# Kernel optimization log

Hardware: AMD Instinct MI355X
Metric: run time of the kernel (lower is better)

## Reference

```python
import jax, jax.numpy as jnp
import numpy as np

EPS = 1e-5
TEMP = 0.07
LARGE_NEG = -1e9


def mi_net(x, W1, g1, b1, W2, b2, Ws, lng, lnb):
    # x: (B, C, T). 1x1 convs == per-position channel projections.
    y = jnp.einsum('bct,oc->bot', x, W1)                      # conv1 (no bias)
    mu = y.mean(axis=(0, 2), keepdims=True)                   # BatchNorm2d, training-mode batch stats
    var = y.var(axis=(0, 2), keepdims=True)
    y = (y - mu) * jax.lax.rsqrt(var + EPS) * g1[None, :, None] + b1[None, :, None]
    y = jax.nn.relu(y)
    y = jnp.einsum('bot,po->bpt', y, W2) + b2[None, :, None]  # conv2 (bias)
    h = y + jnp.einsum('bct,oc->bot', x, Ws)                  # linear shortcut
    mu2 = h.mean(axis=1, keepdims=True)                       # LayerNorm over channel dim
    v2 = h.var(axis=1, keepdims=True)
    return (h - mu2) * jax.lax.rsqrt(v2 + EPS) * lng[None, :, None] + lnb[None, :, None]


def infonce(L, G):
    # L: (N, D, T) locals, G: (N, D) single global per sample (n_multis = 1)
    N, D, T = L.shape
    l_p = jnp.swapaxes(L, 1, 2)                               # (N, T, D)
    l_p = l_p / jnp.linalg.norm(l_p, axis=2, keepdims=True)
    g = G / jnp.linalg.norm(G, axis=1, keepdims=True)         # (N, D)
    u_p = (jnp.einsum('ntd,nd->nt', l_p, g) / TEMP)[:, :, None]   # (N, T, 1), positives scaled by temp
    # negatives: <global_i, local_{j,t}>; NOT divided by temperature (faithful to torch source)
    u_n = jnp.einsum('nd,mtd->nmt', g, l_p)                   # (N, N, T)
    eye = jnp.eye(N, dtype=bool)[:, :, None]
    u_n = jnp.where(eye, LARGE_NEG, u_n).reshape(N, N * T)    # mask self pairs
    logits = jnp.concatenate(
        [u_p, jnp.broadcast_to(u_n[:, None, :], (N, T, N * T))], axis=2)  # (N, T, 1+N*T)
    logp = jax.nn.log_softmax(logits, axis=2)
    return -logp[:, :, 0].mean()


def setup_inputs() -> dict:
    key = jax.random.key(0)
    ks = jax.random.split(key, 10)
    B, CL, CG, T, MI = 32, 1536, 192, 256, 512
    d = {
        'local_feat': jax.random.normal(ks[0], (B, CL, T), jnp.float32),
        'global_feat': jax.random.normal(ks[1], (B, CG), jnp.float32),
        # local_net params
        'lW1': jax.random.normal(ks[2], (MI, CL), jnp.float32) * 0.02,
        'lg1': jnp.ones((MI,), jnp.float32),
        'lb1': jnp.zeros((MI,), jnp.float32),
        'lW2': jax.random.normal(ks[3], (MI, MI), jnp.float32) * 0.02,
        'lb2': jnp.zeros((MI,), jnp.float32),
        'lWs': jax.random.normal(ks[4], (MI, CL), jnp.float32) * 0.02,
        'llng': jnp.ones((MI,), jnp.float32),
        'llnb': jnp.zeros((MI,), jnp.float32),
        # global_net params (global_channels != mi_units -> net exists)
        'gW1': jax.random.normal(ks[5], (MI, CG), jnp.float32) * 0.02,
        'gg1': jnp.ones((MI,), jnp.float32),
        'gb1': jnp.zeros((MI,), jnp.float32),
        'gW2': jax.random.normal(ks[6], (MI, MI), jnp.float32) * 0.02,
        'gb2': jnp.zeros((MI,), jnp.float32),
    }
    # shortcut with near-identity init (n_units >= n_input for global net)
    gWs = jax.random.uniform(ks[7], (MI, CG), jnp.float32, -0.01, 0.01)
    gWs = gWs.at[jnp.arange(CG), jnp.arange(CG)].set(1.0)
    d['gWs'] = gWs
    d['glng'] = jnp.ones((MI,), jnp.float32)
    d['glnb'] = jnp.zeros((MI,), jnp.float32)
    return d


def reference(local_feat, global_feat,
              lW1, lg1, lb1, lW2, lb2, lWs, llng, llnb,
              gW1, gg1, gb1, gW2, gb2, gWs, glng, glnb):
    L = mi_net(local_feat, lW1, lg1, lb1, lW2, lb2, lWs, llng, llnb)      # (B, MI, T)
    G = mi_net(global_feat[:, :, None], gW1, gg1, gb1, gW2, gb2, gWs, glng, glnb)[:, :, 0]  # (B, MI)
    return infonce(L, G)
```

## Files before the change

### kernel.cpp

```cpp
#include <hip/hip_runtime.h>

#define B 32
#define CL 1536
#define CG 192
#define T 256
#define MI 512
#define NPOS 8192
#define EPS 1e-5f
#define TEMP 0.07f

typedef __attribute__((ext_vector_type(8))) __bf16 bf16x8;
typedef __attribute__((ext_vector_type(4))) float f32x4;

__device__ __forceinline__ unsigned short f2bf(float f) {
  union { float f; unsigned u; } v; v.f = f;
  unsigned r = v.u + 0x7FFFu + ((v.u >> 16) & 1u);
  return (unsigned short)(r >> 16);
}
__device__ __forceinline__ float bf2f(unsigned short h) {
  union { unsigned u; float f; } v; v.u = ((unsigned)h) << 16;
  return v.f;
}

__device__ __forceinline__ float wave_sum(float v) {
#pragma unroll
  for (int off = 32; off > 0; off >>= 1) v += __shfl_xor(v, off, 64);
  return v;
}
__device__ __forceinline__ float wave_max(float v) {
#pragma unroll
  for (int off = 32; off > 0; off >>= 1) v = fmaxf(v, __shfl_xor(v, off, 64));
  return v;
}
__device__ __forceinline__ float block_sum(float v, float* rb) {
  v = wave_sum(v);
  __syncthreads();
  if ((threadIdx.x & 63) == 0) rb[threadIdx.x >> 6] = v;
  __syncthreads();
  return rb[0] + rb[1] + rb[2] + rb[3];
}
__device__ __forceinline__ float block_max(float v, float* rb) {
  v = wave_max(v);
  __syncthreads();
  if ((threadIdx.x & 63) == 0) rb[threadIdx.x >> 6] = v;
  __syncthreads();
  return fmaxf(fmaxf(rb[0], rb[1]), fmaxf(rb[2], rb[3]));
}
__device__ __forceinline__ float bs128(float v, float* rb) {
  v = wave_sum(v);
  __syncthreads();
  if ((threadIdx.x & 63) == 0) rb[threadIdx.x >> 6] = v;
  __syncthreads();
  return rb[0] + rb[1];
}

__global__ __launch_bounds__(256) void k_prep(
    const float* __restrict__ x, const float* __restrict__ lW1,
    const float* __restrict__ lWs, const float* __restrict__ lW2,
    const float* __restrict__ gx, const float* __restrict__ gW1,
    unsigned short* __restrict__ xT, unsigned short* __restrict__ Wc,
    unsigned short* __restrict__ W2b, float* __restrict__ y1g,
    float* __restrict__ bsum) {
  __shared__ float xs[64][65];
  const int bi = blockIdx.x, tid = threadIdx.x;
  if (bi < 1792) {
    int idx = (bi * 256 + tid) * 4;
    const float* src; unsigned short* dst;
    if (idx < 786432) { src = lW1 + idx; dst = Wc + idx; }
    else if (idx < 1572864) { src = lWs + (idx - 786432); dst = Wc + idx; }
    else { src = lW2 + (idx - 1572864); dst = W2b + (idx - 1572864); }
    float4 v = *(const float4*)src;
    ushort4 o = {f2bf(v.x), f2bf(v.y), f2bf(v.z), f2bf(v.w)};
    *(ushort4*)dst = o;
  } else if (bi < 4864) {
    int bi2 = bi - 1792;
    int b = bi2 / 96, rem = bi2 - b * 96;
    int c0 = (rem >> 2) * 64, t0 = (rem & 3) * 64;
    const float* xb = x + ((size_t)b * CL + c0) * T + t0;
#pragma unroll
    for (int i = 0; i < 16; i++) {
      int idx = tid + i * 256, c = idx >> 6, t = idx & 63;
      xs[c][t] = xb[(size_t)c * T + t];
    }
    __syncthreads();
    unsigned short* ob = xT + ((size_t)b * T + t0) * CL + c0;
#pragma unroll
    for (int i = 0; i < 8; i++) {
      int idx = tid + i * 256, t = idx >> 5, k = (idx & 31) * 2;
      ushort2 v = {f2bf(xs[k][t]), f2bf(xs[k + 1][t])};
      *(ushort2*)&ob[(size_t)t * CL + k] = v;
    }
  } else if (bi < 4928) {
    int idx = (bi - 4864) * 256 + tid;
    int b = idx & 31, o = idx >> 5;
    float s = 0.f;
    for (int c = 0; c < CG; c++) s = fmaf(gx[b * CG + c], gW1[o * CG + c], s);
    y1g[o * 32 + b] = s;
  } else {
    float4 z = {0.f, 0.f, 0.f, 0.f};
    ((float4*)bsum)[tid] = z;
  }
}

__global__ __launch_bounds__(128, 4) void k_gemm1(
    const unsigned short* __restrict__ xT, const unsigned short* __restrict__ Wc,
    unsigned short* __restrict__ y1u, unsigned short* __restrict__ ysb,
    float* __restrict__ bsum, float* __restrict__ bsq,
    const float* __restrict__ y1g, const float* __restrict__ gg1,
    const float* __restrict__ gb1, float* __restrict__ gscale,
    float* __restrict__ gshift) {
  const int tid = threadIdx.x, bi = blockIdx.x;
  if (bi >= 1024) {
    int o = (bi - 1024) * 128 + tid;
    float s = 0.f, s2 = 0.f;
    for (int b = 0; b < 32; b++) {
      float v = y1g[o * 32 + b];
      s += v; s2 = fmaf(v, v, s2);
    }
    float mu = s * (1.f / 32.f);
    float var = s2 * (1.f / 32.f) - mu * mu;
    float sc = gg1[o] * rsqrtf(var + EPS);
    gscale[o] = sc;
    gshift[o] = gb1[o] - mu * sc;
    return;
  }
  __shared__ __align__(16) unsigned short As[64][32];
  __shared__ __align__(16) unsigned short Bs[128][32];
  __shared__ float ps[128], pq[128];
  const int w = tid >> 6, lane = tid & 63;
  const int m0 = (bi & 127) * 64, o0 = (bi >> 7) * 128;
  const int sr = lane >> 2, sc = (lane & 3) * 8;
  const int lm = lane & 15, q = lane >> 4;
  f32x4 acc[4][4];
#pragma unroll
  for (int i = 0; i < 4; i++)
#pragma unroll
    for (int j = 0; j < 4; j++) acc[i][j] = f32x4{0.f, 0.f, 0.f, 0.f};

  const unsigned short* pa = xT + (size_t)(m0 + w * 32 + sr) * CL + sc;
  const unsigned short* pb = Wc + (size_t)(o0 + w * 64 + sr) * CL + sc;
  for (int k0 = 0; k0 < CL; k0 += 32) {
    __builtin_amdgcn_global_load_lds(
        (const __attribute__((address_space(1))) void*)(pa + k0),
        (__attribute__((address_space(3))) void*)&As[w * 32][0], 16, 0, 0);
    __builtin_amdgcn_global_load_lds(
        (const __attribute__((address_space(1))) void*)(pa + 16 * CL + k0),
        (__attribute__((address_space(3))) void*)&As[w * 32 + 16][0], 16, 0, 0);
    __builtin_amdgcn_global_load_lds(
        (const __attribute__((address_space(1))) void*)(pb + k0),
        (__attribute__((address_space(3))) void*)&Bs[w * 64][0], 16, 0, 0);
    __builtin_amdgcn_global_load_lds(
        (const __attribute__((address_space(1))) void*)(pb + 16 * CL + k0),
        (__attribute__((address_space(3))) void*)&Bs[w * 64 + 16][0], 16, 0, 0);
    __builtin_amdgcn_global_load_lds(
        (const __attribute__((address_space(1))) void*)(pb + 32 * CL + k0),
        (__attribute__((address_space(3))) void*)&Bs[w * 64 + 32][0], 16, 0, 0);
    __builtin_amdgcn_global_load_lds(
        (const __attribute__((address_space(1))) void*)(pb + 48 * CL + k0),
        (__attribute__((address_space(3))) void*)&Bs[w * 64 + 48][0], 16, 0, 0);
    __syncthreads();
    bf16x8 af[4], bfr[4];
#pragma unroll
    for (int mi = 0; mi < 4; mi++)
      af[mi] = *(const bf16x8*)&As[mi * 16 + lm][q * 8];
#pragma unroll
    for (int ni = 0; ni < 4; ni++)
      bfr[ni] = *(const bf16x8*)&Bs[w * 64 + ni * 16 + lm][q * 8];
#pragma unroll
    for (int mi = 0; mi < 4; mi++)
#pragma unroll
      for (int ni = 0; ni < 4; ni++)
        acc[mi][ni] = __builtin_amdgcn_mfma_f32_16x16x32_bf16(
            af[mi], bfr[ni], acc[mi][ni], 0, 0, 0);
    __syncthreads();
  }
  const int row0 = m0 + q * 4;
  const bool isY1 = (o0 < 512);
  unsigned short* dst = isY1 ? y1u : ysb;
  const int ob = isY1 ? o0 : o0 - 512;
#pragma unroll
  for (int mi = 0; mi < 4; mi++)
#pragma unroll
    for (int ni = 0; ni < 4; ni++) {
      int oc = ob + w * 64 + ni * 16 + lm;
#pragma unroll
      for (int r = 0; r < 4; r++)
        dst[(size_t)(row0 + mi * 16 + r) * 512 + oc] = f2bf(acc[mi][ni][r]);
    }
  if (isY1) {
#pragma unroll
    for (int ni = 0; ni < 4; ni++) {
      float s = 0.f, s2 = 0.f;
#pragma unroll
      for (int mi = 0; mi < 4; mi++)
#pragma unroll
        for (int r = 0; r < 4; r++) {
          float v = acc[mi][ni][r];
          s += v; s2 = fmaf(v, v, s2);
        }
      s += __shfl_xor(s, 16, 64);  s2 += __shfl_xor(s2, 16, 64);
      s += __shfl_xor(s, 32, 64);  s2 += __shfl_xor(s2, 32, 64);
      if (q == 0) {
        int c = w * 64 + ni * 16 + lm;
        ps[c] = s; pq[c] = s2;
      }
    }
    __syncthreads();
    atomicAdd(&bsum[o0 + tid], ps[tid]);
    atomicAdd(&bsq[o0 + tid], pq[tid]);
  }
}

__global__ __launch_bounds__(256) void k_bnapp(
    const unsigned short* __restrict__ y1u, const float* __restrict__ bsum,
    const float* __restrict__ bsq, const float* __restrict__ lg1,
    const float* __restrict__ lb1, unsigned short* __restrict__ vv,
    const float* __restrict__ y1g, const float* __restrict__ gscale,
    const float* __restrict__ gshift, const float* __restrict__ gW2,
    const float* __restrict__ gb2, const float* __restrict__ gx,
    const float* __restrict__ gWsc, float* __restrict__ hg) {
  const int bi = blockIdx.x, tid = threadIdx.x;
  if (bi < 4096) {
    int idx = (bi * 256 + tid) * 4;
    int o = idx & 511;
    ushort4 in = *(const ushort4*)&y1u[idx];
    float iv[4] = {bf2f(in.x), bf2f(in.y), bf2f(in.z), bf2f(in.w)};
    unsigned short ov[4];
#pragma unroll
    for (int j = 0; j < 4; j++) {
      float mu = bsum[o + j] * (1.f / NPOS);
      float var = bsq[o + j] * (1.f / NPOS) - mu * mu;
      float sc = lg1[o + j] * rsqrtf(var + EPS);
      float sh = lb1[o + j] - mu * sc;
      ov[j] = f2bf(fmaxf(fmaf(iv[j], sc, sh), 0.f));
    }
    ushort4 out = {ov[0], ov[1], ov[2], ov[3]};
    *(ushort4*)&vv[idx] = out;
  } else {
    int idx = (bi - 4096) * 256 + tid;
    int b = idx & 31, p = idx >> 5;
    float s = gb2[p];
    for (int o = 0; o < MI; o++) {
      float v = fmaxf(fmaf(y1g[o * 32 + b], gscale[o], gshift[o]), 0.f);
      s = fmaf(v, gW2[(size_t)p * MI + o], s);
    }
    for (int c = 0; c < CG; c++) s = fmaf(gx[b * CG + c], gWsc[p * CG + c], s);
    hg[p * 32 + b] = s;
  }
}

__global__ __launch_bounds__(128, 4) void k_gemm2(
    const unsigned short* __restrict__ vv, const unsigned short* __restrict__ W2b,
    const float* __restrict__ b2, const unsigned short* __restrict__ ysb,
    unsigned short* __restrict__ hb16,
    const float* __restrict__ hg, const float* __restrict__ glng,
    const float* __restrict__ glnb, unsigned short* __restrict__ gnormb) {
  __shared__ __align__(16) unsigned short As[64][32];
  __shared__ __align__(16) unsigned short Bs[128][32];
  __shared__ float rb[2];
  const int tid = threadIdx.x, bi = blockIdx.x;
  if (bi >= 512) {
    int b = bi - 512;
    float v[4], Lv[4];
    float s = 0.f, s2 = 0.f;
#pragma unroll
    for (int j = 0; j < 4; j++) {
      v[j] = hg[(tid + j * 128) * 32 + b];
      s += v[j]; s2 = fmaf(v[j], v[j], s2);
    }
    s = bs128(s, rb);
    s2 = bs128(s2, rb);
    float mu = s * (1.f / MI);
    float var = s2 * (1.f / MI) - mu * mu;
    float rstd = rsqrtf(var + EPS);
    float n2 = 0.f;
#pragma unroll
    for (int j = 0; j < 4; j++) {
      int p = tid + j * 128;
      Lv[j] = fmaf((v[j] - mu) * rstd, glng[p], glnb[p]);
      n2 = fmaf(Lv[j], Lv[j], n2);
    }
    n2 = bs128(n2, rb);
    float inv = rsqrtf(n2);
#pragma unroll
    for (int j = 0; j < 4; j++)
      gnormb[b * MI + tid + j * 128] = f2bf(Lv[j] * inv);
    return;
  }
  const int w = tid >> 6, lane = tid & 63;
  const int m0 = (bi & 127) * 64, p0 = (bi >> 7) * 128;
  const int sr = lane >> 2, sc = (lane & 3) * 8;
  const int lm = lane & 15, q = lane >> 4;
  f32x4 acc[4][4];
#pragma unroll
  for (int i = 0; i < 4; i++)
#pragma unroll
    for (int j = 0; j < 4; j++) acc[i][j] = f32x4{0.f, 0.f, 0.f, 0.f};

  const unsigned short* pa = vv + (size_t)(m0 + w * 32 + sr) * 512 + sc;
  const unsigned short* pb = W2b + (size_t)(p0 + w * 64 + sr) * 512 + sc;
  for (int k0 = 0; k0 < 512; k0 += 32) {
    __builtin_amdgcn_global_load_lds(
        (const __attribute__((address_space(1))) void*)(pa + k0),
        (__attribute__((address_space(3))) void*)&As[w * 32][0], 16, 0, 0);
    __builtin_amdgcn_global_load_lds(
        (const __attribute__((address_space(1))) void*)(pa + 16 * 512 + k0),
        (__attribute__((address_space(3))) void*)&As[w * 32 + 16][0], 16, 0, 0);
    __builtin_amdgcn_global_load_lds(
        (const __attribute__((address_space(1))) void*)(pb + k0),
        (__attribute__((address_space(3))) void*)&Bs[w * 64][0], 16, 0, 0);
    __builtin_amdgcn_global_load_lds(
        (const __attribute__((address_space(1))) void*)(pb + 16 * 512 + k0),
        (__attribute__((address_space(3))) void*)&Bs[w * 64 + 16][0], 16, 0, 0);
    __builtin_amdgcn_global_load_lds(
        (const __attribute__((address_space(1))) void*)(pb + 32 * 512 + k0),
        (__attribute__((address_space(3))) void*)&Bs[w * 64 + 32][0], 16, 0, 0);
    __builtin_amdgcn_global_load_lds(
        (const __attribute__((address_space(1))) void*)(pb + 48 * 512 + k0),
        (__attribute__((address_space(3))) void*)&Bs[w * 64 + 48][0], 16, 0, 0);
    __syncthreads();
    bf16x8 af[4], bfr[4];
#pragma unroll
    for (int mi = 0; mi < 4; mi++)
      af[mi] = *(const bf16x8*)&As[mi * 16 + lm][q * 8];
#pragma unroll
    for (int ni = 0; ni < 4; ni++)
      bfr[ni] = *(const bf16x8*)&Bs[w * 64 + ni * 16 + lm][q * 8];
#pragma unroll
    for (int mi = 0; mi < 4; mi++)
#pragma unroll
      for (int ni = 0; ni < 4; ni++)
        acc[mi][ni] = __builtin_amdgcn_mfma_f32_16x16x32_bf16(
            af[mi], bfr[ni], acc[mi][ni], 0, 0, 0);
    __syncthreads();
  }
  const int row0 = m0 + q * 4;
#pragma unroll
  for (int ni = 0; ni < 4; ni++) {
    int p = p0 + w * 64 + ni * 16 + lm;
    float bias = b2[p];
#pragma unroll
    for (int mi = 0; mi < 4; mi++)
#pragma unroll
      for (int r = 0; r < 4; r++) {
        size_t off = (size_t)(row0 + mi * 16 + r) * 512 + p;
        hb16[off] = f2bf(acc[mi][ni][r] + bias + bf2f(ysb[off]));
      }
  }
}

__global__ __launch_bounds__(256) void k_ln(
    const unsigned short* __restrict__ hb16, const float* __restrict__ lng,
    const float* __restrict__ lnb, unsigned short* __restrict__ Lb) {
  const int tid = threadIdx.x;
  const int r = blockIdx.x * 4 + (tid >> 6), lane = tid & 63;
  const unsigned short* row = hb16 + (size_t)r * 512 + lane * 8;
  ushort4 u0 = *(const ushort4*)row;
  ushort4 u1 = *(const ushort4*)(row + 4);
  float v[8] = {bf2f(u0.x), bf2f(u0.y), bf2f(u0.z), bf2f(u0.w),
                bf2f(u1.x), bf2f(u1.y), bf2f(u1.z), bf2f(u1.w)};
  float s = 0.f, s2 = 0.f;
#pragma unroll
  for (int j = 0; j < 8; j++) { s += v[j]; s2 = fmaf(v[j], v[j], s2); }
  s = wave_sum(s);
  s2 = wave_sum(s2);
  float mu = s * (1.f / MI);
  float var = s2 * (1.f / MI) - mu * mu;
  float rstd = rsqrtf(var + EPS);
  float4 g0 = *(const float4*)&lng[lane * 8];
  float4 g1 = *(const float4*)&lng[lane * 8 + 4];
  float4 bb0 = *(const float4*)&lnb[lane * 8];
  float4 bb1 = *(const float4*)&lnb[lane * 8 + 4];
  float gg[8] = {g0.x, g0.y, g0.z, g0.w, g1.x, g1.y, g1.z, g1.w};
  float bz[8] = {bb0.x, bb0.y, bb0.z, bb0.w, bb1.x, bb1.y, bb1.z, bb1.w};
  float L[8], n2 = 0.f;
#pragma unroll
  for (int j = 0; j < 8; j++) {
    L[j] = fmaf((v[j] - mu) * rstd, gg[j], bz[j]);
    n2 = fmaf(L[j], L[j], n2);
  }
  n2 = wave_sum(n2);
  float inv = rsqrtf(n2);
  unsigned short* orow = Lb + (size_t)r * 512 + lane * 8;
  ushort4 o0 = {f2bf(L[0] * inv), f2bf(L[1] * inv), f2bf(L[2] * inv), f2bf(L[3] * inv)};
  ushort4 o1 = {f2bf(L[4] * inv), f2bf(L[5] * inv), f2bf(L[6] * inv), f2bf(L[7] * inv)};
  *(ushort4*)orow = o0;
  *(ushort4*)(orow + 4) = o1;
}

__global__ __launch_bounds__(256) void k_u(
    const unsigned short* __restrict__ g, const unsigned short* __restrict__ Lb,
    float* __restrict__ U) {
  const int tid = threadIdx.x;
  const int w = tid >> 6, lane = tid & 63;
  const int lm = lane & 15, q = lane >> 4;
  const int rbase = blockIdx.x * 128 + w * 32;
  f32x4 acc[2][2];
#pragma unroll
  for (int i = 0; i < 2; i++)
#pragma unroll
    for (int j = 0; j < 2; j++) acc[i][j] = f32x4{0.f, 0.f, 0.f, 0.f};
  for (int k0 = 0; k0 < 512; k0 += 32) {
    bf16x8 af[2], bfr[2];
#pragma unroll
    for (int mi = 0; mi < 2; mi++)
      af[mi] = *(const bf16x8*)&g[(size_t)(mi * 16 + lm) * 512 + k0 + q * 8];
#pragma unroll
    for (int ni = 0; ni < 2; ni++)
      bfr[ni] = *(const bf16x8*)&Lb[(size_t)(rbase + ni * 16 + lm) * 512 + k0 + q * 8];
#pragma unroll
    for (int mi = 0; mi < 2; mi++)
#pragma unroll
      for (int ni = 0; ni < 2; ni++)
        acc[mi][ni] = __builtin_amdgcn_mfma_f32_16x16x32_bf16(
            af[mi], bfr[ni], acc[mi][ni], 0, 0, 0);
  }
#pragma unroll
  for (int mi = 0; mi < 2; mi++)
#pragma unroll
    for (int ni = 0; ni < 2; ni++) {
      int row = rbase + ni * 16 + lm;
#pragma unroll
      for (int r = 0; r < 4; r++) {
        int gi = mi * 16 + q * 4 + r;
        U[(size_t)gi * NPOS + row] = acc[mi][ni][r];
      }
    }
}

__global__ __launch_bounds__(256) void k_rowstats(
    const float* __restrict__ U, float* __restrict__ pmax, float* __restrict__ psum) {
  __shared__ float rb[4];
  const int n = blockIdx.y, c = blockIdx.x, tid = threadIdx.x;
  float4 v = ((const float4*)(U + (size_t)n * NPOS + c * 1024))[tid];
  int m = (c * 1024 + tid * 4) >> 8;
  if (m == n) { v.x = v.y = v.z = v.w = -1e30f; }
  float mx = fmaxf(fmaxf(v.x, v.y), fmaxf(v.z, v.w));
  mx = block_max(mx, rb);
  float s = expf(v.x - mx) + expf(v.y - mx) + expf(v.z - mx) + expf(v.w - mx);
  s = block_sum(s, rb);
  if (tid == 0) { pmax[n * 8 + c] = mx; psum[n * 8 + c] = s; }
}

__global__ __launch_bounds__(256) void k_loss(
    const float* __restrict__ U, const float* __restrict__ pmax,
    const float* __restrict__ psum, float* __restrict__ out) {
  __shared__ float rb[4];
  __shared__ float cm[32], cs[32];
  const int tid = threadIdx.x;
  if (tid < 32) {
    float M = -1e30f;
#pragma unroll
    for (int c = 0; c < 8; c++) M = fmaxf(M, pmax[tid * 8 + c]);
    float S = 0.f;
#pragma unroll
    for (int c = 0; c < 8; c++) S += psum[tid * 8 + c] * expf(pmax[tid * 8 + c] - M);
    cm[tid] = M; cs[tid] = S;
  }
  __syncthreads();
  float s = 0.f;
  for (int i = tid; i < NPOS; i += 256) {
    int n = i >> 8, t = i & 255;
    float up = U[(size_t)n * NPOS + n * T + t] * (1.f / TEMP);
    float M = cm[n], S = cs[n];
    float mx = fmaxf(up, M);
    float lse = mx + logf(expf(up - mx) + S * expf(M - mx));
    s += lse - up;
  }
  s = block_sum(s, rb);
  if (tid == 0) out[0] = s * (1.f / NPOS);
}

extern "C" void kernel_launch(void* const* d_in, const int* in_sizes, int n_in,
                              void* d_out, int out_size, void* d_ws, size_t ws_size,
                              hipStream_t stream) {
  (void)in_sizes; (void)n_in; (void)out_size; (void)ws_size;
  const float* x    = (const float*)d_in[0];
  const float* gx   = (const float*)d_in[1];
  const float* lW1  = (const float*)d_in[2];
  const float* lg1  = (const float*)d_in[3];
  const float* lb1  = (const float*)d_in[4];
  const float* lW2  = (const float*)d_in[5];
  const float* lb2  = (const float*)d_in[6];
  const float* lWs  = (const float*)d_in[7];
  const float* llng = (const float*)d_in[8];
  const float* llnb = (const float*)d_in[9];
  const float* gW1  = (const float*)d_in[10];
  const float* gg1  = (const float*)d_in[11];
  const float* gb1  = (const float*)d_in[12];
  const float* gW2  = (const float*)d_in[13];
  const float* gb2  = (const float*)d_in[14];
  const float* gWs  = (const float*)d_in[15];
  const float* glng = (const float*)d_in[16];
  const float* glnb = (const float*)d_in[17];

  char* wsb = (char*)d_ws;
  unsigned short* xT     = (unsigned short*)(wsb);
  unsigned short* Wc     = (unsigned short*)(wsb + 25165824);
  unsigned short* W2b    = (unsigned short*)(wsb + 28311552);
  unsigned short* y1u    = (unsigned short*)(wsb + 28835840);
  unsigned short* ysb    = (unsigned short*)(wsb + 37224448);
  unsigned short* vv     = (unsigned short*)(wsb + 45613056);
  unsigned short* hb16   = (unsigned short*)(wsb + 54001664);
  unsigned short* Lb     = (unsigned short*)(wsb + 62390272);
  float* U               = (float*)(wsb + 70778880);
  float* bsum            = (float*)(wsb + 71827456);
  float* bsq             = (float*)(wsb + 71829504);
  float* y1g             = (float*)(wsb + 71831552);
  float* gscale          = (float*)(wsb + 71897088);
  float* gshift          = (float*)(wsb + 71899136);
  float* hg              = (float*)(wsb + 71901184);
  unsigned short* gnormb = (unsigned short*)(wsb + 71966720);
  float* pmax            = (float*)(wsb + 71999488);
  float* psum            = (float*)(wsb + 72000512);

  k_prep<<<dim3(4929), 256, 0, stream>>>(x, lW1, lWs, lW2, gx, gW1, xT, Wc, W2b,
                                         y1g, bsum);
  k_gemm1<<<dim3(1028), 128, 0, stream>>>(xT, Wc, y1u, ysb, bsum, bsq,
                                          y1g, gg1, gb1, gscale, gshift);
  k_bnapp<<<dim3(4160), 256, 0, stream>>>(y1u, bsum, bsq, lg1, lb1, vv,
                                          y1g, gscale, gshift, gW2, gb2, gx, gWs, hg);
  k_gemm2<<<dim3(544), 128, 0, stream>>>(vv, W2b, lb2, ysb, hb16,
                                         hg, glng, glnb, gnormb);
  k_ln<<<dim3(2048), 256, 0, stream>>>(hb16, llng, llnb, Lb);
  k_u<<<dim3(64), 256, 0, stream>>>(gnormb, Lb, U);
  k_rowstats<<<dim3(8, 32), 256, 0, stream>>>(U, pmax, psum);
  k_loss<<<dim3(1), 256, 0, stream>>>(U, pmax, psum, (float*)d_out);
}
```

Before: 248.8 us.

## Halve GEMM N-tiles, move global-net path into gemm1, fuse LN/U/rowstats tail

Both bf16 GEMMs now use 64x64 tiles instead of 64x128, which doubles the block count so more CUs are busy. The global-net BatchNorm and second projection move out of k_bnapp into extra blocks of k_gemm1, with the scale and shift kept in shared memory. LayerNorm, the U GEMM and the per-row softmax statistics are fused into one k_tail kernel that never writes the full U or the normalized locals to global memory, and k_loss now reduces 256 partials per row. Smaller tiles mean less data reuse per block, and the fused tail runs only 256 blocks with heavy shared-memory use.

```diff
diff --git a/kernel.cpp b/kernel.cpp
--- a/kernel.cpp
+++ b/kernel.cpp
@@ -27,24 +27,12 @@
   for (int off = 32; off > 0; off >>= 1) v += __shfl_xor(v, off, 64);
   return v;
 }
-__device__ __forceinline__ float wave_max(float v) {
-#pragma unroll
-  for (int off = 32; off > 0; off >>= 1) v = fmaxf(v, __shfl_xor(v, off, 64));
-  return v;
-}
 __device__ __forceinline__ float block_sum(float v, float* rb) {
   v = wave_sum(v);
   __syncthreads();
   if ((threadIdx.x & 63) == 0) rb[threadIdx.x >> 6] = v;
   __syncthreads();
   return rb[0] + rb[1] + rb[2] + rb[3];
-}
-__device__ __forceinline__ float block_max(float v, float* rb) {
-  v = wave_max(v);
-  __syncthreads();
-  if ((threadIdx.x & 63) == 0) rb[threadIdx.x >> 6] = v;
-  __syncthreads();
-  return fmaxf(fmaxf(rb[0], rb[1]), fmaxf(rb[2], rb[3]));
 }
 __device__ __forceinline__ float bs128(float v, float* rb) {
   v = wave_sum(v);
@@ -107,38 +95,57 @@
     unsigned short* __restrict__ y1u, unsigned short* __restrict__ ysb,
     float* __restrict__ bsum, float* __restrict__ bsq,
     const float* __restrict__ y1g, const float* __restrict__ gg1,
-    const float* __restrict__ gb1, float* __restrict__ gscale,
-    float* __restrict__ gshift) {
+    const float* __restrict__ gb1, const float* __restrict__ gW2,
+    const float* __restrict__ gb2, const float* __restrict__ gx,
+    const float* __restrict__ gWsc, float* __restrict__ hg) {
   const int tid = threadIdx.x, bi = blockIdx.x;
-  if (bi >= 1024) {
-    int o = (bi - 1024) * 128 + tid;
-    float s = 0.f, s2 = 0.f;
-    for (int b = 0; b < 32; b++) {
-      float v = y1g[o * 32 + b];
-      s += v; s2 = fmaf(v, v, s2);
-    }
-    float mu = s * (1.f / 32.f);
-    float var = s2 * (1.f / 32.f) - mu * mu;
-    float sc = gg1[o] * rsqrtf(var + EPS);
-    gscale[o] = sc;
-    gshift[o] = gb1[o] - mu * sc;
+  if (bi >= 2048) {
+    __shared__ float gsc[512], gsh[512];
+#pragma unroll
+    for (int jj = 0; jj < 4; jj++) {
+      int o = tid + jj * 128;
+      float s = 0.f, s2 = 0.f;
+      for (int b = 0; b < 32; b++) {
+        float v = y1g[o * 32 + b];
+        s += v; s2 = fmaf(v, v, s2);
+      }
+      float mu = s * (1.f / 32.f);
+      float var = s2 * (1.f / 32.f) - mu * mu;
+      float sc = gg1[o] * rsqrtf(var + EPS);
+      gsc[o] = sc;
+      gsh[o] = gb1[o] - mu * sc;
+    }
+    __syncthreads();
+    int base = (bi - 2048) * 256;
+#pragma unroll
+    for (int jj = 0; jj < 2; jj++) {
+      int idx = base + jj * 128 + tid;
+      int b = idx & 31, p = idx >> 5;
+      float s = gb2[p];
+      for (int o = 0; o < MI; o++) {
+        float v = fmaxf(fmaf(y1g[o * 32 + b], gsc[o], gsh[o]), 0.f);
+        s = fmaf(v, gW2[(size_t)p * MI + o], s);
+      }
+      for (int c = 0; c < CG; c++) s = fmaf(gx[b * CG + c], gWsc[p * CG + c], s);
+      hg[p * 32 + b] = s;
+    }
     return;
   }
   __shared__ __align__(16) unsigned short As[64][32];
-  __shared__ __align__(16) unsigned short Bs[128][32];
-  __shared__ float ps[128], pq[128];
+  __shared__ __align__(16) unsigned short Bs[64][32];
+  __shared__ float ps[64], pq[64];
   const int w = tid >> 6, lane = tid & 63;
-  const int m0 = (bi & 127) * 64, o0 = (bi >> 7) * 128;
+  const int m0 = (bi & 127) * 64, o0 = (bi >> 7) * 64;
   const int sr = lane >> 2, sc = (lane & 3) * 8;
   const int lm = lane & 15, q = lane >> 4;
-  f32x4 acc[4][4];
+  f32x4 acc[4][2];
 #pragma unroll
   for (int i = 0; i < 4; i++)
 #pragma unroll
-    for (int j = 0; j < 4; j++) acc[i][j] = f32x4{0.f, 0.f, 0.f, 0.f};
+    for (int j = 0; j < 2; j++) acc[i][j] = f32x4{0.f, 0.f, 0.f, 0.f};
 
   const unsigned short* pa = xT + (size_t)(m0 + w * 32 + sr) * CL + sc;
-  const unsigned short* pb = Wc + (size_t)(o0 + w * 64 + sr) * CL + sc;
+  const unsigned short* pb = Wc + (size_t)(o0 + w * 32 + sr) * CL + sc;
   for (int k0 = 0; k0 < CL; k0 += 32) {
     __builtin_amdgcn_global_load_lds(
         (const __attribute__((address_space(1))) void*)(pa + k0),
@@ -148,28 +155,22 @@
         (__attribute__((address_space(3))) void*)&As[w * 32 + 16][0], 16, 0, 0);
     __builtin_amdgcn_global_load_lds(
         (const __attribute__((address_space(1))) void*)(pb + k0),
-        (__attribute__((address_space(3))) void*)&Bs[w * 64][0], 16, 0, 0);
+        (__attribute__((address_space(3))) void*)&Bs[w * 32][0], 16, 0, 0);
     __builtin_amdgcn_global_load_lds(
         (const __attribute__((address_space(1))) void*)(pb + 16 * CL + k0),
-        (__attribute__((address_space(3))) void*)&Bs[w * 64 + 16][0], 16, 0, 0);
-    __builtin_amdgcn_global_load_lds(
-        (const __attribute__((address_space(1))) void*)(pb + 32 * CL + k0),
-        (__attribute__((address_space(3))) void*)&Bs[w * 64 + 32][0], 16, 0, 0);
-    __builtin_amdgcn_global_load_lds(
-        (const __attribute__((address_space(1))) void*)(pb + 48 * CL + k0),
-        (__attribute__((address_space(3))) void*)&Bs[w * 64 + 48][0], 16, 0, 0);
-    __syncthreads();
-    bf16x8 af[4], bfr[4];
+        (__attribute__((address_space(3))) void*)&Bs[w * 32 + 16][0], 16, 0, 0);
+    __syncthreads();
+    bf16x8 af[4], bfr[2];
 #pragma unroll
     for (int mi = 0; mi < 4; mi++)
       af[mi] = *(const bf16x8*)&As[mi * 16 + lm][q * 8];
 #pragma unroll
-    for (int ni = 0; ni < 4; ni++)
-      bfr[ni] = *(const bf16x8*)&Bs[w * 64 + ni * 16 + lm][q * 8];
+    for (int ni = 0; ni < 2; ni++)
+      bfr[ni] = *(const bf16x8*)&Bs[w * 32 + ni * 16 + lm][q * 8];
 #pragma unroll
     for (int mi = 0; mi < 4; mi++)
 #pragma unroll
-      for (int ni = 0; ni < 4; ni++)
+      for (int ni = 0; ni < 2; ni++)
         acc[mi][ni] = __builtin_amdgcn_mfma_f32_16x16x32_bf16(
             af[mi], bfr[ni], acc[mi][ni], 0, 0, 0);
     __syncthreads();
@@ -181,15 +182,15 @@
 #pragma unroll
   for (int mi = 0; mi < 4; mi++)
 #pragma unroll
-    for (int ni = 0; ni < 4; ni++) {
-      int oc = ob + w * 64 + ni * 16 + lm;
+    for (int ni = 0; ni < 2; ni++) {
+      int oc = ob + w * 32 + ni * 16 + lm;
 #pragma unroll
       for (int r = 0; r < 4; r++)
         dst[(size_t)(row0 + mi * 16 + r) * 512 + oc] = f2bf(acc[mi][ni][r]);
     }
   if (isY1) {
 #pragma unroll
-    for (int ni = 0; ni < 4; ni++) {
+    for (int ni = 0; ni < 2; ni++) {
       float s = 0.f, s2 = 0.f;
 #pragma unroll
       for (int mi = 0; mi < 4; mi++)
@@ -201,52 +202,37 @@
       s += __shfl_xor(s, 16, 64);  s2 += __shfl_xor(s2, 16, 64);
       s += __shfl_xor(s, 32, 64);  s2 += __shfl_xor(s2, 32, 64);
       if (q == 0) {
-        int c = w * 64 + ni * 16 + lm;
+        int c = w * 32 + ni * 16 + lm;
         ps[c] = s; pq[c] = s2;
       }
     }
     __syncthreads();
-    atomicAdd(&bsum[o0 + tid], ps[tid]);
-    atomicAdd(&bsq[o0 + tid], pq[tid]);
+    if (tid < 64) {
+      atomicAdd(&bsum[o0 + tid], ps[tid]);
+      atomicAdd(&bsq[o0 + tid], pq[tid]);
+    }
   }
 }
 
 __global__ __launch_bounds__(256) void k_bnapp(
     const unsigned short* __restrict__ y1u, const float* __restrict__ bsum,
     const float* __restrict__ bsq, const float* __restrict__ lg1,
-    const float* __restrict__ lb1, unsigned short* __restrict__ vv,
-    const float* __restrict__ y1g, const float* __restrict__ gscale,
-    const float* __restrict__ gshift, const float* __restrict__ gW2,
-    const float* __restrict__ gb2, const float* __restrict__ gx,
-    const float* __restrict__ gWsc, float* __restrict__ hg) {
-  const int bi = blockIdx.x, tid = threadIdx.x;
-  if (bi < 4096) {
-    int idx = (bi * 256 + tid) * 4;
-    int o = idx & 511;
-    ushort4 in = *(const ushort4*)&y1u[idx];
-    float iv[4] = {bf2f(in.x), bf2f(in.y), bf2f(in.z), bf2f(in.w)};
-    unsigned short ov[4];
-#pragma unroll
-    for (int j = 0; j < 4; j++) {
-      float mu = bsum[o + j] * (1.f / NPOS);
-      float var = bsq[o + j] * (1.f / NPOS) - mu * mu;
-      float sc = lg1[o + j] * rsqrtf(var + EPS);
-      float sh = lb1[o + j] - mu * sc;
-      ov[j] = f2bf(fmaxf(fmaf(iv[j], sc, sh), 0.f));
-    }
-    ushort4 out = {ov[0], ov[1], ov[2], ov[3]};
-    *(ushort4*)&vv[idx] = out;
-  } else {
-    int idx = (bi - 4096) * 256 + tid;
-    int b = idx & 31, p = idx >> 5;
-    float s = gb2[p];
-    for (int o = 0; o < MI; o++) {
-      float v = fmaxf(fmaf(y1g[o * 32 + b], gscale[o], gshift[o]), 0.f);
-      s = fmaf(v, gW2[(size_t)p * MI + o], s);
-    }
-    for (int c = 0; c < CG; c++) s = fmaf(gx[b * CG + c], gWsc[p * CG + c], s);
-    hg[p * 32 + b] = s;
-  }
+    const float* __restrict__ lb1, unsigned short* __restrict__ vv) {
+  int idx = (blockIdx.x * 256 + threadIdx.x) * 4;
+  int o = idx & 511;
+  ushort4 in = *(const ushort4*)&y1u[idx];
+  float iv[4] = {bf2f(in.x), bf2f(in.y), bf2f(in.z), bf2f(in.w)};
+  unsigned short ov[4];
+#pragma unroll
+  for (int j = 0; j < 4; j++) {
+    float mu = bsum[o + j] * (1.f / NPOS);
+    float var = bsq[o + j] * (1.f / NPOS) - mu * mu;
+    float sc = lg1[o + j] * rsqrtf(var + EPS);
+    float sh = lb1[o + j] - mu * sc;
+    ov[j] = f2bf(fmaxf(fmaf(iv[j], sc, sh), 0.f));
+  }
+  ushort4 out = {ov[0], ov[1], ov[2], ov[3]};
+  *(ushort4*)&vv[idx] = out;
 }
 
 __global__ __launch_bounds__(128, 4) void k_gemm2(
@@ -256,11 +242,11 @@
     const float* __restrict__ hg, const float* __restrict__ glng,
     const float* __restrict__ glnb, unsigned short* __restrict__ gnormb) {
   __shared__ __align__(16) unsigned short As[64][32];
-  __shared__ __align__(16) unsigned short Bs[128][32];
+  __shared__ __align__(16) unsigned short Bs[64][32];
   __shared__ float rb[2];
   const int tid = threadIdx.x, bi = blockIdx.x;
-  if (bi >= 512) {
-    int b = bi - 512;
+  if (bi >= 1024) {
+    int b = bi - 1024;
     float v[4], Lv[4];
     float s = 0.f, s2 = 0.f;
 #pragma unroll
@@ -288,17 +274,17 @@
     return;
   }
   const int w = tid >> 6, lane = tid & 63;
-  const int m0 = (bi & 127) * 64, p0 = (bi >> 7) * 128;
+  const int m0 = (bi & 127) * 64, p0 = (bi >> 7) * 64;
   const int sr = lane >> 2, sc = (lane & 3) * 8;
   const int lm = lane & 15, q = lane >> 4;
-  f32x4 acc[4][4];
+  f32x4 acc[4][2];
 #pragma unroll
   for (int i = 0; i < 4; i++)
 #pragma unroll
-    for (int j = 0; j < 4; j++) acc[i][j] = f32x4{0.f, 0.f, 0.f, 0.f};
+    for (int j = 0; j < 2; j++) acc[i][j] = f32x4{0.f, 0.f, 0.f, 0.f};
 
   const unsigned short* pa = vv + (size_t)(m0 + w * 32 + sr) * 512 + sc;
-  const unsigned short* pb = W2b + (size_t)(p0 + w * 64 + sr) * 512 + sc;
+  const unsigned short* pb = W2b + (size_t)(p0 + w * 32 + sr) * 512 + sc;
   for (int k0 = 0; k0 < 512; k0 += 32) {
     __builtin_amdgcn_global_load_lds(
         (const __attribute__((address_space(1))) void*)(pa + k0),
@@ -308,36 +294,30 @@
         (__attribute__((address_space(3))) void*)&As[w * 32 + 16][0], 16, 0, 0);
     __builtin_amdgcn_global_load_lds(
         (const __attribute__((address_space(1))) void*)(pb + k0),
-        (__attribute__((address_space(3))) void*)&Bs[w * 64][0], 16, 0, 0);
+        (__attribute__((address_space(3))) void*)&Bs[w * 32][0], 16, 0, 0);
     __builtin_amdgcn_global_load_lds(
         (const __attribute__((address_space(1))) void*)(pb + 16 * 512 + k0),
-        (__attribute__((address_space(3))) void*)&Bs[w * 64 + 16][0], 16, 0, 0);
-    __builtin_amdgcn_global_load_lds(
-        (const __attribute__((address_space(1))) void*)(pb + 32 * 512 + k0),
-        (__attribute__((address_space(3))) void*)&Bs[w * 64 + 32][0], 16, 0, 0);
-    __builtin_amdgcn_global_load_lds(
-        (const __attribute__((address_space(1))) void*)(pb + 48 * 512 + k0),
-        (__attribute__((address_space(3))) void*)&Bs[w * 64 + 48][0], 16, 0, 0);
-    __syncthreads();
-    bf16x8 af[4], bfr[4];
+        (__attribute__((address_space(3))) void*)&Bs[w * 32 + 16][0], 16, 0, 0);
+    __syncthreads();
+    bf16x8 af[4], bfr[2];
 #pragma unroll
     for (int mi = 0; mi < 4; mi++)
       af[mi] = *(const bf16x8*)&As[mi * 16 + lm][q * 8];
 #pragma unroll
-    for (int ni = 0; ni < 4; ni++)
-      bfr[ni] = *(const bf16x8*)&Bs[w * 64 + ni * 16 + lm][q * 8];
+    for (int ni = 0; ni < 2; ni++)
+      bfr[ni] = *(const bf16x8*)&Bs[w * 32 + ni * 16 + lm][q * 8];
 #pragma unroll
     for (int mi = 0; mi < 4; mi++)
 #pragma unroll
-      for (int ni = 0; ni < 4; ni++)
+      for (int ni = 0; ni < 2; ni++)
         acc[mi][ni] = __builtin_amdgcn_mfma_f32_16x16x32_bf16(
             af[mi], bfr[ni], acc[mi][ni], 0, 0, 0);
     __syncthreads();
   }
   const int row0 = m0 + q * 4;
 #pragma unroll
-  for (int ni = 0; ni < 4; ni++) {
-    int p = p0 + w * 64 + ni * 16 + lm;
+  for (int ni = 0; ni < 2; ni++) {
+    int p = p0 + w * 32 + ni * 16 + lm;
     float bias = b2[p];
 #pragma unroll
     for (int mi = 0; mi < 4; mi++)
@@ -349,65 +329,75 @@
   }
 }
 
-__global__ __launch_bounds__(256) void k_ln(
+__global__ __launch_bounds__(256) void k_tail(
     const unsigned short* __restrict__ hb16, const float* __restrict__ lng,
-    const float* __restrict__ lnb, unsigned short* __restrict__ Lb) {
+    const float* __restrict__ lnb, const unsigned short* __restrict__ gnormb,
+    float* __restrict__ up, float* __restrict__ pmax, float* __restrict__ psum) {
+  __shared__ __align__(16) unsigned short gs[32 * 512];
+  __shared__ __align__(16) unsigned short Ls[32 * 512];
+  __shared__ float Ured[4 * 1024];
   const int tid = threadIdx.x;
-  const int r = blockIdx.x * 4 + (tid >> 6), lane = tid & 63;
-  const unsigned short* row = hb16 + (size_t)r * 512 + lane * 8;
-  ushort4 u0 = *(const ushort4*)row;
-  ushort4 u1 = *(const ushort4*)(row + 4);
-  float v[8] = {bf2f(u0.x), bf2f(u0.y), bf2f(u0.z), bf2f(u0.w),
-                bf2f(u1.x), bf2f(u1.y), bf2f(u1.z), bf2f(u1.w)};
-  float s = 0.f, s2 = 0.f;
-#pragma unroll
-  for (int j = 0; j < 8; j++) { s += v[j]; s2 = fmaf(v[j], v[j], s2); }
-  s = wave_sum(s);
-  s2 = wave_sum(s2);
-  float mu = s * (1.f / MI);
-  float var = s2 * (1.f / MI) - mu * mu;
-  float rstd = rsqrtf(var + EPS);
+  const int w = tid >> 6, lane = tid & 63;
+  const int r0 = blockIdx.x * 32;
+  const int smp = r0 >> 8;
+#pragma unroll
+  for (int i = 0; i < 8; i++) {
+    int e = (tid + i * 256) * 8;
+    *(uint4*)&gs[e] = *(const uint4*)&gnormb[e];
+  }
   float4 g0 = *(const float4*)&lng[lane * 8];
   float4 g1 = *(const float4*)&lng[lane * 8 + 4];
   float4 bb0 = *(const float4*)&lnb[lane * 8];
   float4 bb1 = *(const float4*)&lnb[lane * 8 + 4];
   float gg[8] = {g0.x, g0.y, g0.z, g0.w, g1.x, g1.y, g1.z, g1.w};
   float bz[8] = {bb0.x, bb0.y, bb0.z, bb0.w, bb1.x, bb1.y, bb1.z, bb1.w};
-  float L[8], n2 = 0.f;
 #pragma unroll
   for (int j = 0; j < 8; j++) {
-    L[j] = fmaf((v[j] - mu) * rstd, gg[j], bz[j]);
-    n2 = fmaf(L[j], L[j], n2);
-  }
-  n2 = wave_sum(n2);
-  float inv = rsqrtf(n2);
-  unsigned short* orow = Lb + (size_t)r * 512 + lane * 8;
-  ushort4 o0 = {f2bf(L[0] * inv), f2bf(L[1] * inv), f2bf(L[2] * inv), f2bf(L[3] * inv)};
-  ushort4 o1 = {f2bf(L[4] * inv), f2bf(L[5] * inv), f2bf(L[6] * inv), f2bf(L[7] * inv)};
-  *(ushort4*)orow = o0;
-  *(ushort4*)(orow + 4) = o1;
-}
-
-__global__ __launch_bounds__(256) void k_u(
-    const unsigned short* __restrict__ g, const unsigned short* __restrict__ Lb,
-    float* __restrict__ U) {
-  const int tid = threadIdx.x;
-  const int w = tid >> 6, lane = tid & 63;
+    int rr = w * 8 + j;
+    const unsigned short* row = hb16 + (size_t)(r0 + rr) * 512 + lane * 8;
+    ushort4 u0 = *(const ushort4*)row;
+    ushort4 u1 = *(const ushort4*)(row + 4);
+    float v[8] = {bf2f(u0.x), bf2f(u0.y), bf2f(u0.z), bf2f(u0.w),
+                  bf2f(u1.x), bf2f(u1.y), bf2f(u1.z), bf2f(u1.w)};
+    float s = 0.f, s2 = 0.f;
+#pragma unroll
+    for (int k = 0; k < 8; k++) { s += v[k]; s2 = fmaf(v[k], v[k], s2); }
+    s = wave_sum(s);
+    s2 = wave_sum(s2);
+    float mu = s * (1.f / MI);
+    float var = s2 * (1.f / MI) - mu * mu;
+    float rstd = rsqrtf(var + EPS);
+    float L[8], n2 = 0.f;
+#pragma unroll
+    for (int k = 0; k < 8; k++) {
+      L[k] = fmaf((v[k] - mu) * rstd, gg[k], bz[k]);
+      n2 = fmaf(L[k], L[k], n2);
+    }
+    n2 = wave_sum(n2);
+    float inv = rsqrtf(n2);
+    unsigned short* orow = &Ls[rr * 512 + lane * 8];
+    ushort4 o0 = {f2bf(L[0] * inv), f2bf(L[1] * inv), f2bf(L[2] * inv), f2bf(L[3] * inv)};
+    ushort4 o1 = {f2bf(L[4] * inv), f2bf(L[5] * inv), f2bf(L[6] * inv), f2bf(L[7] * inv)};
+    *(ushort4*)orow = o0;
+    *(ushort4*)(orow + 4) = o1;
+  }
+  __syncthreads();
   const int lm = lane & 15, q = lane >> 4;
-  const int rbase = blockIdx.x * 128 + w * 32;
   f32x4 acc[2][2];
 #pragma unroll
   for (int i = 0; i < 2; i++)
 #pragma unroll
     for (int j = 0; j < 2; j++) acc[i][j] = f32x4{0.f, 0.f, 0.f, 0.f};
-  for (int k0 = 0; k0 < 512; k0 += 32) {
+#pragma unroll
+  for (int kk = 0; kk < 4; kk++) {
+    int k0 = w * 128 + kk * 32 + q * 8;
     bf16x8 af[2], bfr[2];
 #pragma unroll
     for (int mi = 0; mi < 2; mi++)
-      af[mi] = *(const bf16x8*)&g[(size_t)(mi * 16 + lm) * 512 + k0 + q * 8];
+      af[mi] = *(const bf16x8*)&gs[(mi * 16 + lm) * 512 + k0];
 #pragma unroll
     for (int ni = 0; ni < 2; ni++)
-      bfr[ni] = *(const bf16x8*)&Lb[(size_t)(rbase + ni * 16 + lm) * 512 + k0 + q * 8];
+      bfr[ni] = *(const bf16x8*)&Ls[(ni * 16 + lm) * 512 + k0];
 #pragma unroll
     for (int mi = 0; mi < 2; mi++)
 #pragma unroll
@@ -418,57 +408,84 @@
 #pragma unroll
   for (int mi = 0; mi < 2; mi++)
 #pragma unroll
-    for (int ni = 0; ni < 2; ni++) {
-      int row = rbase + ni * 16 + lm;
+    for (int ni = 0; ni < 2; ni++)
 #pragma unroll
       for (int r = 0; r < 4; r++) {
-        int gi = mi * 16 + q * 4 + r;
-        U[(size_t)gi * NPOS + row] = acc[mi][ni][r];
+        int m = mi * 16 + q * 4 + r, n = ni * 16 + lm;
+        Ured[w * 1024 + m * 32 + n] = acc[mi][ni][r];
       }
-    }
-}
-
-__global__ __launch_bounds__(256) void k_rowstats(
-    const float* __restrict__ U, float* __restrict__ pmax, float* __restrict__ psum) {
-  __shared__ float rb[4];
-  const int n = blockIdx.y, c = blockIdx.x, tid = threadIdx.x;
-  float4 v = ((const float4*)(U + (size_t)n * NPOS + c * 1024))[tid];
-  int m = (c * 1024 + tid * 4) >> 8;
-  if (m == n) { v.x = v.y = v.z = v.w = -1e30f; }
-  float mx = fmaxf(fmaxf(v.x, v.y), fmaxf(v.z, v.w));
-  mx = block_max(mx, rb);
-  float s = expf(v.x - mx) + expf(v.y - mx) + expf(v.z - mx) + expf(v.w - mx);
-  s = block_sum(s, rb);
-  if (tid == 0) { pmax[n * 8 + c] = mx; psum[n * 8 + c] = s; }
+  __syncthreads();
+  float u[4];
+#pragma unroll
+  for (int j = 0; j < 4; j++) {
+    int idx = tid * 4 + j;
+    u[j] = Ured[idx] + Ured[1024 + idx] + Ured[2048 + idx] + Ured[3072 + idx];
+  }
+  __syncthreads();
+#pragma unroll
+  for (int j = 0; j < 4; j++) Ured[tid * 4 + j] = u[j];
+  int m = (tid * 4) >> 5;
+  if (m == smp) {
+#pragma unroll
+    for (int j = 0; j < 4; j++)
+      up[r0 + ((tid * 4 + j) & 31)] = u[j] * (1.f / TEMP);
+  }
+  __syncthreads();
+  if (tid < 32) {
+    float mx = -1e30f, s = 0.f;
+    if (tid != smp) {
+      for (int n = 0; n < 32; n++) mx = fmaxf(mx, Ured[tid * 32 + n]);
+      for (int n = 0; n < 32; n++) s += expf(Ured[tid * 32 + n] - mx);
+    }
+    pmax[tid * 256 + blockIdx.x] = mx;
+    psum[tid * 256 + blockIdx.x] = s;
+  }
 }
 
 __global__ __launch_bounds__(256) void k_loss(
-    const float* __restrict__ U, const float* __restrict__ pmax,
+    const float* __restrict__ up, const float* __restrict__ pmax,
     const float* __restrict__ psum, float* __restrict__ out) {
   __shared__ float rb[4];
-  __shared__ float cm[32], cs[32];
+  __shared__ float red[32][8];
+  __shared__ float Ms[32], Ss[32];
   const int tid = threadIdx.x;
-  if (tid < 32) {
+  const int n = tid >> 3, j = tid & 7;
+  float mx = -1e30f;
+  for (int c = j * 32; c < j * 32 + 32; c++) mx = fmaxf(mx, pmax[n * 256 + c]);
+  red[n][j] = mx;
+  __syncthreads();
+  if (j == 0) {
     float M = -1e30f;
 #pragma unroll
-    for (int c = 0; c < 8; c++) M = fmaxf(M, pmax[tid * 8 + c]);
+    for (int k = 0; k < 8; k++) M = fmaxf(M, red[n][k]);
+    Ms[n] = M;
+  }
+  __syncthreads();
+  float M = Ms[n];
+  float s = 0.f;
+  for (int c = j * 32; c < j * 32 + 32; c++)
+    s += psum[n * 256 + c] * expf(pmax[n * 256 + c] - M);
+  __syncthreads();
+  red[n][j] = s;
+  __syncthreads();
+  if (j == 0) {
     float S = 0.f;
 #pragma unroll
-    for (int c = 0; c < 8; c++) S += psum[tid * 8 + c] * expf(pmax[tid * 8 + c] - M);
-    cm[tid] = M; cs[tid] = S;
-  }
-  __syncthreads();
-  float s = 0.f;
+    for (int k = 0; k < 8; k++) S += red[n][k];
+    Ss[n] = S;
+  }
+  __syncthreads();
+  float acc = 0.f;
   for (int i = tid; i < NPOS; i += 256) {
-    int n = i >> 8, t = i & 255;
-    float up = U[(size_t)n * NPOS + n * T + t] * (1.f / TEMP);
-    float M = cm[n], S = cs[n];
-    float mx = fmaxf(up, M);
-    float lse = mx + logf(expf(up - mx) + S * expf(M - mx));
-    s += lse - up;
-  }
-  s = block_sum(s, rb);
-  if (tid == 0) out[0] = s * (1.f / NPOS);
+    int nn = i >> 8;
+    float upv = up[i];
+    float Mn = Ms[nn], Sn = Ss[nn];
+    float mx2 = fmaxf(upv, Mn);
+    float lse = mx2 + logf(expf(upv - mx2) + Sn * expf(Mn - mx2));
+    acc += lse - upv;
+  }
+  acc = block_sum(acc, rb);
+  if (tid == 0) out[0] = acc * (1.f / NPOS);
 }
 
 extern "C" void kernel_launch(void* const* d_in, const int* in_sizes, int n_in,
@@ -502,28 +519,22 @@
   unsigned short* ysb    = (unsigned short*)(wsb + 37224448);
   unsigned short* vv     = (unsigned short*)(wsb + 45613056);
   unsigned short* hb16   = (unsigned short*)(wsb + 54001664);
-  unsigned short* Lb     = (unsigned short*)(wsb + 62390272);
-  float* U               = (float*)(wsb + 70778880);
   float* bsum            = (float*)(wsb + 71827456);
   float* bsq             = (float*)(wsb + 71829504);
   float* y1g             = (float*)(wsb + 71831552);
-  float* gscale          = (float*)(wsb + 71897088);
-  float* gshift          = (float*)(wsb + 71899136);
   float* hg              = (float*)(wsb + 71901184);
   unsigned short* gnormb = (unsigned short*)(wsb + 71966720);
-  float* pmax            = (float*)(wsb + 71999488);
-  float* psum            = (float*)(wsb + 72000512);
+  float* up              = (float*)(wsb + 71999488);
+  float* pmax            = (float*)(wsb + 72032256);
+  float* psum            = (float*)(wsb + 72065024);
 
   k_prep<<<dim3(4929), 256, 0, stream>>>(x, lW1, lWs, lW2, gx, gW1, xT, Wc, W2b,
                                          y1g, bsum);
-  k_gemm1<<<dim3(1028), 128, 0, stream>>>(xT, Wc, y1u, ysb, bsum, bsq,
-                                          y1g, gg1, gb1, gscale, gshift);
-  k_bnapp<<<dim3(4160), 256, 0, stream>>>(y1u, bsum, bsq, lg1, lb1, vv,
-                                          y1g, gscale, gshift, gW2, gb2, gx, gWs, hg);
-  k_gemm2<<<dim3(544), 128, 0, stream>>>(vv, W2b, lb2, ysb, hb16,
-                                         hg, glng, glnb, gnormb);
-  k_ln<<<dim3(2048), 256, 0, stream>>>(hb16, llng, llnb, Lb);
-  k_u<<<dim3(64), 256, 0, stream>>>(gnormb, Lb, U);
-  k_rowstats<<<dim3(8, 32), 256, 0, stream>>>(U, pmax, psum);
-  k_loss<<<dim3(1), 256, 0, stream>>>(U, pmax, psum, (float*)d_out);
-}
+  k_gemm1<<<dim3(2112), 128, 0, stream>>>(xT, Wc, y1u, ysb, bsum, bsq,
+                                          y1g, gg1, gb1, gW2, gb2, gx, gWs, hg);
+  k_bnapp<<<dim3(4096), 256, 0, stream>>>(y1u, bsum, bsq, lg1, lb1, vv);
+  k_gemm2<<<dim3(1056), 128, 0, stream>>>(vv, W2b, lb2, ysb, hb16,
+                                          hg, glng, glnb, gnormb);
+  k_tail<<<dim3(256), 256, 0, stream>>>(hb16, llng, llnb, gnormb, up, pmax, psum);
+  k_loss<<<dim3(1), 256, 0, stream>>>(up, pmax, psum, (float*)d_out);
+}
```

Result: slower. 254.2 us (+2.2%).
